# Kernel optimization log

Measured on AMD Instinct MI355X. Metric: run time of the kernel, lower is better.

## Reference

```python
import jax, jax.numpy as jnp
import numpy as np

NUM_HEAD = 16
D_MODEL = 1024


def setup_inputs() -> dict:
    key = jax.random.key(0)
    k1, k2, k3 = jax.random.split(key, 3)
    B, S = 4, 2048
    x = jax.random.normal(k1, (B, S, D_MODEL), dtype=jnp.float32)
    W_qkv = jax.random.normal(k2, (D_MODEL, 3 * D_MODEL), dtype=jnp.float32) * (D_MODEL ** -0.5)
    b_qkv = jnp.zeros((3 * D_MODEL,), dtype=jnp.float32)
    W_o = jax.random.normal(k3, (D_MODEL, D_MODEL), dtype=jnp.float32) * (D_MODEL ** -0.5)
    b_o = jnp.zeros((D_MODEL,), dtype=jnp.float32)
    return {"x": x, "W_qkv": W_qkv, "b_qkv": b_qkv, "W_o": W_o, "b_o": b_o}


def reference(x, W_qkv, b_qkv, W_o, b_o):
    B, S, dm = x.shape
    H = NUM_HEAD
    hd = dm // H
    qkv = x @ W_qkv + b_qkv                       # [B,S,3*dm]
    qkv = qkv.reshape(B, S, H, 3 * hd).transpose(0, 2, 1, 3)  # [B,H,S,3*hd]
    q, k, v = jnp.split(qkv, 3, axis=-1)          # each [B,H,S,hd]
    scale = jnp.sqrt(jnp.asarray(hd, dtype=q.dtype))
    att = jnp.einsum('bhqd,bhkd->bhqk', q, k) / scale  # [B,H,S,S]
    causal = jnp.tril(jnp.ones((S, S), dtype=bool))    # band_part(ones,-1,0)
    att = jnp.where(causal, att, -jnp.inf)             # additive 0 / -inf mask
    att = jax.nn.softmax(att, axis=-1)
    vals = jnp.einsum('bhqk,bhkd->bhqd', att, v)       # [B,H,S,hd]
    # Faithful to original: reshape WITHOUT transposing heads back (axis scramble)
    vals = vals.reshape(B, S, H * hd)
    return vals @ W_o + b_o
```

## Files before the change

kernel.cpp:

```cpp
#include <hip/hip_runtime.h>
#include <hip/hip_bf16.h>
#include <stdint.h>


typedef __attribute__((ext_vector_type(8))) __bf16 bf16x8;
typedef __attribute__((ext_vector_type(4))) float f32x4;
typedef __attribute__((ext_vector_type(16))) float f32x16;

#define AS_G __attribute__((address_space(1)))
#define AS_L __attribute__((address_space(3)))

__device__ __forceinline__ void gload_lds16(const void* g, void* s) {
  __builtin_amdgcn_global_load_lds((const AS_G void*)g, (AS_L void*)s, 16, 0, 0);
}

__device__ __forceinline__ unsigned cvt_pk_bf16(float lo, float hi) {
  unsigned r;
  asm("v_cvt_pk_bf16_f32 %0, %1, %2" : "=v"(r) : "v"(lo), "v"(hi));
  return r;
}

__global__ void cvt_bf16_kernel(const float* __restrict__ in,
                                __bf16* __restrict__ out, int n8) {
  int i = blockIdx.x * blockDim.x + threadIdx.x;
  if (i >= n8) return;
  float4 a = ((const float4*)in)[i * 2];
  float4 b = ((const float4*)in)[i * 2 + 1];
  union { __bf16 h[8]; int4 v; } u;
  u.h[0] = (__bf16)a.x; u.h[1] = (__bf16)a.y; u.h[2] = (__bf16)a.z; u.h[3] = (__bf16)a.w;
  u.h[4] = (__bf16)b.x; u.h[5] = (__bf16)b.y; u.h[6] = (__bf16)b.z; u.h[7] = (__bf16)b.w;
  ((int4*)out)[i] = u.v;
}

__global__ void cvt_T_kernel(const float* __restrict__ in,
                             __bf16* __restrict__ out, int K, int N) {
  __shared__ float tile[32][33];
  int bx = blockIdx.x;
  int by = blockIdx.y;
  int tx = threadIdx.x & 31, ty = threadIdx.x >> 5;
#pragma unroll
  for (int i = 0; i < 32; i += 8)
    tile[ty + i][tx] = in[(size_t)(by * 32 + ty + i) * N + bx * 32 + tx];
  __syncthreads();
#pragma unroll
  for (int i = 0; i < 32; i += 8)
    out[(size_t)(bx * 32 + ty + i) * K + by * 32 + tx] = (__bf16)tile[tx][ty + i];
}

template <int MODE, int NT, int MCHUNK>
__global__ __launch_bounds__(256, 2) void gemm_bt(
    const __bf16* __restrict__ A, const __bf16* __restrict__ Bt,
    const float* __restrict__ bias,
    __bf16* __restrict__ Qb, __bf16* __restrict__ Kb, __bf16* __restrict__ Vtb,
    float* __restrict__ Out) {
  __shared__ char lds[65536];
  const int tid = threadIdx.x;
  const int wave = tid >> 6, lane = tid & 63;
  const int lhi = lane >> 4, llo = lane & 15;
  const int wm = wave >> 1, wn = wave & 1;

  const int wg = blockIdx.x + blockIdx.y * gridDim.x;
  const int xcd = wg & 7, local = wg >> 3;
  const int m0 = (xcd * MCHUNK + (local & (MCHUNK - 1))) * 128;
  const int n0 = (local / MCHUNK) * 128;

  int S[2];
#pragma unroll
  for (int j = 0; j < 2; ++j) {
    const int idx = j * 256 + tid;
    const int v = idx >> 3, wl = idx & 7;
    const int wg_ = wl ^ (v & 7);
    const int r = (v << 1) | (wg_ >> 2), u2 = wg_ & 3;
    S[j] = r * 1024 + u2 * 8;
  }
  const __bf16* Asrc = A + (size_t)m0 * 1024;
  const __bf16* Bsrc = Bt + (size_t)n0 * 1024;
  const int dstw = wave * 1024;

  auto stageAB = [&](int c, int t, int ks) {
    char* ab = &lds[c * 16384 + ks * 8192];
    char* bb = &lds[32768 + c * 16384 + ks * 8192];
    const int go = t * 64 + ks * 32;
    gload_lds16(Asrc + S[0] + go, ab + dstw);
    gload_lds16(Asrc + S[1] + go, ab + 4096 + dstw);
    gload_lds16(Bsrc + S[0] + go, bb + dstw);
    gload_lds16(Bsrc + S[1] + go, bb + 4096 + dstw);
  };

  f32x4 acc[4][4];
#pragma unroll
  for (int mi = 0; mi < 4; ++mi)
#pragma unroll
    for (int nj = 0; nj < 4; ++nj) acc[mi][nj] = (f32x4){0.f, 0.f, 0.f, 0.f};

  auto aoff = [&](int c, int ks, int mi) {
    const int r = wm * 64 + mi * 16 + llo;
    const int v = r >> 1;
    const int w = ((r & 1) << 2) | lhi;
    return c * 16384 + ks * 8192 + v * 128 + ((w ^ (v & 7)) << 4);
  };
  auto boff = [&](int c, int ks, int nj) {
    const int r = wn * 64 + nj * 16 + llo;
    const int v = r >> 1;
    const int w = ((r & 1) << 2) | lhi;
    return 32768 + c * 16384 + ks * 8192 + v * 128 + ((w ^ (v & 7)) << 4);
  };

  auto phase = [&](int c, int ks, int sc, int st, int sks) {
    bf16x8 fa[4], fb[4];
#pragma unroll
    for (int mi = 0; mi < 4; ++mi) fa[mi] = *(const bf16x8*)&lds[aoff(c, ks, mi)];
#pragma unroll
    for (int nj = 0; nj < 4; ++nj) fb[nj] = *(const bf16x8*)&lds[boff(c, ks, nj)];
    stageAB(sc, st, sks);
    __builtin_amdgcn_sched_barrier(0);
    asm volatile("s_waitcnt vmcnt(8)" ::: "memory");
    __builtin_amdgcn_sched_barrier(0);
    __builtin_amdgcn_s_barrier();
    __builtin_amdgcn_s_setprio(1);
#pragma unroll
    for (int mi = 0; mi < 4; ++mi)
#pragma unroll
      for (int nj = 0; nj < 4; ++nj)
        acc[mi][nj] = __builtin_amdgcn_mfma_f32_16x16x32_bf16(fa[mi], fb[nj],
                                                              acc[mi][nj], 0, 0, 0);
    __builtin_amdgcn_s_setprio(0);
    __builtin_amdgcn_sched_barrier(0);
    __builtin_amdgcn_s_barrier();
  };

  stageAB(0, 0, 0);
  stageAB(0, 0, 1);
  stageAB(1, 1, 0);
  __builtin_amdgcn_sched_barrier(0);
  asm volatile("s_waitcnt vmcnt(8)" ::: "memory");
  __builtin_amdgcn_sched_barrier(0);
  __builtin_amdgcn_s_barrier();

  for (int it = 0; it < 8; ++it) {
    const int T = 2 * it;
    phase(0, 0, 1, (T + 1) & 15, 1);
    phase(0, 1, 0, (T + 2) & 15, 0);
    phase(1, 0, 0, (T + 2) & 15, 1);
    phase(1, 1, 1, (T + 3) & 15, 0);
  }

#pragma unroll
  for (int nj = 0; nj < 4; ++nj) {
    const int col = n0 + wn * 64 + nj * 16 + llo;
    const float bv = bias[col];
    if (MODE == 0) {
      const int h = col / 192, rem = col % 192;
#pragma unroll
      for (int mi = 0; mi < 4; ++mi) {
        const int row0 = m0 + wm * 64 + mi * 16 + lhi * 4;
        const int b = row0 >> 11;
        const int s0 = row0 & 2047;
        const int bh = b * 16 + h;
        f32x4 v = acc[mi][nj];
        if (rem < 64) {
#pragma unroll
          for (int r = 0; r < 4; ++r)
            Qb[((size_t)bh * 2048 + s0 + r) * 64 + rem] =
                (__bf16)((v[r] + bv) * 0.18033688011112042f);
        } else if (rem < 128) {
#pragma unroll
          for (int r = 0; r < 4; ++r)
            Kb[((size_t)bh * 2048 + s0 + r) * 64 + (rem - 64)] = (__bf16)(v[r] + bv);
        } else {
          union { __bf16 h4[4]; int2 v2; } u;
#pragma unroll
          for (int r = 0; r < 4; ++r) u.h4[r] = (__bf16)(v[r] + bv);
          *(int2*)&Vtb[((size_t)bh * 64 + (rem - 128)) * 2048 + s0] = u.v2;
        }
      }
    } else {
#pragma unroll
      for (int mi = 0; mi < 4; ++mi) {
        const int row0 = m0 + wm * 64 + mi * 16 + lhi * 4;
        f32x4 v = acc[mi][nj];
#pragma unroll
        for (int r = 0; r < 4; ++r)
          Out[(size_t)(row0 + r) * 1024 + col] = v[r] + bv;
      }
    }
  }
}


__device__ __forceinline__ void attn_tile(
    const __bf16* __restrict__ ksb, const __bf16* __restrict__ vsb,
    const bf16x8* qf, int kv0, int q0w, int lq, int hi,
    f32x16& o0, f32x16& o1, float& m, float& l) {
  const int r0 = lq, r1 = 32 + lq;
  const int fx = (lq & 7) ^ ((lq >> 3) << 1);
  f32x16 s0, s1;
#pragma unroll
  for (int i = 0; i < 16; ++i) { s0[i] = 0.f; s1[i] = 0.f; }
  __builtin_amdgcn_s_setprio(1);
#pragma unroll
  for (int ds = 0; ds < 4; ++ds) {
    const int bb = ((ds * 2 + hi) ^ fx) * 8;
    bf16x8 k0 = *(const bf16x8*)&ksb[r0 * 64 + bb];
    bf16x8 k1 = *(const bf16x8*)&ksb[r1 * 64 + bb];
    s0 = __builtin_amdgcn_mfma_f32_32x32x16_bf16(k0, qf[ds], s0, 0, 0, 0);
    s1 = __builtin_amdgcn_mfma_f32_32x32x16_bf16(k1, qf[ds], s1, 0, 0, 0);
  }
  __builtin_amdgcn_s_setprio(0);

  const int qg = q0w + lq;
  if (kv0 + 63 > q0w) {
#pragma unroll
    for (int reg = 0; reg < 16; ++reg) {
      const int kvl = (reg & 3) + 8 * (reg >> 2) + 4 * hi;
      if (kv0 + kvl > qg) s0[reg] = -1e30f;
      if (kv0 + 32 + kvl > qg) s1[reg] = -1e30f;
    }
  }
  float x[8];
#pragma unroll
  for (int i = 0; i < 8; ++i)
    x[i] = fmaxf(fmaxf(s0[i], s0[i + 8]), fmaxf(s1[i], s1[i + 8]));
#pragma unroll
  for (int st = 4; st; st >>= 1)
#pragma unroll
    for (int i = 0; i < st; ++i) x[i] = fmaxf(x[i], x[i + st]);
  const float mx = fmaxf(x[0], __shfl_xor(x[0], 32));

  if (!__all(mx <= m + 8.f)) {
    const float mn = fmaxf(m, mx);
    const float f = __builtin_amdgcn_exp2f(m - mn);
    m = mn;
    l *= f;
#pragma unroll
    for (int i = 0; i < 16; ++i) { o0[i] *= f; o1[i] *= f; }
  }
#pragma unroll
  for (int i = 0; i < 16; ++i) s0[i] = __builtin_amdgcn_exp2f(s0[i] - m);
#pragma unroll
  for (int i = 0; i < 16; ++i) s1[i] = __builtin_amdgcn_exp2f(s1[i] - m);
  float y[8];
#pragma unroll
  for (int i = 0; i < 8; ++i) y[i] = (s0[i] + s0[i + 8]) + (s1[i] + s1[i + 8]);
#pragma unroll
  for (int st = 4; st; st >>= 1)
#pragma unroll
    for (int i = 0; i < st; ++i) y[i] += y[i + st];
  l += y[0] + __shfl_xor(y[0], 32);

#pragma unroll
  for (int ks = 0; ks < 4; ++ks) {
    unsigned pa, pb, pc, pd;
    if (ks < 2) {
      pa = cvt_pk_bf16(s0[ks * 8 + 0], s0[ks * 8 + 1]);
      pb = cvt_pk_bf16(s0[ks * 8 + 2], s0[ks * 8 + 3]);
      pc = cvt_pk_bf16(s0[ks * 8 + 4], s0[ks * 8 + 5]);
      pd = cvt_pk_bf16(s0[ks * 8 + 6], s0[ks * 8 + 7]);
    } else {
      pa = cvt_pk_bf16(s1[(ks - 2) * 8 + 0], s1[(ks - 2) * 8 + 1]);
      pb = cvt_pk_bf16(s1[(ks - 2) * 8 + 2], s1[(ks - 2) * 8 + 3]);
      pc = cvt_pk_bf16(s1[(ks - 2) * 8 + 4], s1[(ks - 2) * 8 + 5]);
      pd = cvt_pk_bf16(s1[(ks - 2) * 8 + 6], s1[(ks - 2) * 8 + 7]);
    }
    asm volatile("v_permlane32_swap_b32 %0, %1" : "+v"(pa), "+v"(pc));
    asm volatile("v_permlane32_swap_b32 %0, %1" : "+v"(pb), "+v"(pd));
    union { unsigned u[4]; bf16x8 v; } pf;
    pf.u[0] = pa; pf.u[1] = pb; pf.u[2] = pc; pf.u[3] = pd;
    const int vb = ((ks * 2 + hi) ^ fx) * 8;
    bf16x8 v0 = *(const bf16x8*)&vsb[r0 * 64 + vb];
    bf16x8 v1 = *(const bf16x8*)&vsb[r1 * 64 + vb];
    o0 = __builtin_amdgcn_mfma_f32_32x32x16_bf16(v0, pf.v, o0, 0, 0, 0);
    o1 = __builtin_amdgcn_mfma_f32_32x32x16_bf16(v1, pf.v, o1, 0, 0, 0);
  }
}

__device__ __forceinline__ void attn_epilogue(
    __bf16* __restrict__ vals, int bh, int q0w, int lq, int hi,
    const f32x16& o0, const f32x16& o1, float l) {
  const float inv = 1.f / l;
  unsigned* outp = (unsigned*)(vals + ((size_t)bh * 2048 + q0w + lq) * 64);
#pragma unroll
  for (int n = 0; n < 2; ++n) {
#pragma unroll
    for (int g = 0; g < 2; ++g) {
      const float e0 = (n ? o1[g * 8 + 0] : o0[g * 8 + 0]) * inv;
      const float e1 = (n ? o1[g * 8 + 1] : o0[g * 8 + 1]) * inv;
      const float e2 = (n ? o1[g * 8 + 2] : o0[g * 8 + 2]) * inv;
      const float e3 = (n ? o1[g * 8 + 3] : o0[g * 8 + 3]) * inv;
      const float e4 = (n ? o1[g * 8 + 4] : o0[g * 8 + 4]) * inv;
      const float e5 = (n ? o1[g * 8 + 5] : o0[g * 8 + 5]) * inv;
      const float e6 = (n ? o1[g * 8 + 6] : o0[g * 8 + 6]) * inv;
      const float e7 = (n ? o1[g * 8 + 7] : o0[g * 8 + 7]) * inv;
      unsigned a = cvt_pk_bf16(e0, e1);
      unsigned a2 = cvt_pk_bf16(e2, e3);
      unsigned b = cvt_pk_bf16(e4, e5);
      unsigned b2 = cvt_pk_bf16(e6, e7);
      asm volatile("v_permlane32_swap_b32 %0, %1" : "+v"(a), "+v"(b));
      asm volatile("v_permlane32_swap_b32 %0, %1" : "+v"(a2), "+v"(b2));
      int4 st = {(int)a, (int)a2, (int)b, (int)b2};
      *(int4*)&outp[(n * 32 + g * 16 + hi * 8) >> 1] = st;
    }
  }
}

__global__ __launch_bounds__(256) void attn_kernel(
    const __bf16* __restrict__ Q, const __bf16* __restrict__ K,
    const __bf16* __restrict__ Vt, __bf16* __restrict__ vals) {
  __shared__ __bf16 Ks[2][4096];
  __shared__ __bf16 Vs[2][4096];
  const int tid = threadIdx.x;
  const int wave = tid >> 6, lane = tid & 63;
  const int lq = lane & 31, hi = lane >> 5;

  const int wg = blockIdx.x + (blockIdx.y << 3);
  const int wgid = (wg & 7) * 128 + (wg >> 3);
  const int local = wgid & 127;
  const int bh = (wgid >> 7) * 8 + (local & 7);
  const int qc = 15 - (local >> 3);
  const int q0w = qc * 128 + wave * 32;
  const int nt = 2 * qc + 2;

  bf16x8 qf[4];
  {
    const __bf16* qp = Q + ((size_t)bh * 2048 + q0w + lq) * 64 + hi * 8;
#pragma unroll
    for (int ds = 0; ds < 4; ++ds) qf[ds] = *(const bf16x8*)(qp + ds * 16);
  }

  f32x16 o0, o1;
#pragma unroll
  for (int i = 0; i < 16; ++i) { o0[i] = 0.f; o1[i] = 0.f; }
  float m = -3e38f, l = 0.f;

  const int sr = tid >> 3, sb_ = tid & 7;
  const int sc = (sb_ ^ ((sr & 7) ^ ((sr >> 3) << 1))) * 8;
  const __bf16* Kg0 = K + ((size_t)bh * 2048 + sr) * 64 + sc;
  const __bf16* Kg1 = Kg0 + 32 * 64;
  const __bf16* Vg0 = Vt + ((size_t)bh * 64 + sr) * 2048 + sc;
  const __bf16* Vg1 = Vg0 + 32 * 2048;
  __bf16* KsW = &Ks[0][0] + wave * 512;
  __bf16* VsW = &Vs[0][0] + wave * 512;

#define STAGE(buf, t)                                                   \
  gload_lds16(Kg0 + (size_t)(t) * 4096, KsW + (buf) * 4096);            \
  gload_lds16(Kg1 + (size_t)(t) * 4096, KsW + (buf) * 4096 + 2048);     \
  gload_lds16(Vg0 + (t) * 64, VsW + (buf) * 4096);                      \
  gload_lds16(Vg1 + (t) * 64, VsW + (buf) * 4096 + 2048);

  STAGE(0, 0);
  __syncthreads();

  for (int t = 0; t < nt; ++t) {
    const int cur = t & 1;
    if (t + 1 < nt) { STAGE(cur ^ 1, t + 1); }
    attn_tile(&Ks[cur][0], &Vs[cur][0], qf, t * 64, q0w, lq, hi, o0, o1, m, l);
    __syncthreads();
  }
#undef STAGE

  attn_epilogue(vals, bh, q0w, lq, hi, o0, o1, l);
}

extern "C" void kernel_launch(void* const* d_in, const int* in_sizes, int n_in,
                              void* d_out, int out_size, void* d_ws, size_t ws_size,
                              hipStream_t stream) {
  const float* x = (const float*)d_in[0];
  const float* Wqkv = (const float*)d_in[1];
  const float* bqkv = (const float*)d_in[2];
  const float* Wo = (const float*)d_in[3];
  const float* bo = (const float*)d_in[4];
  float* out = (float*)d_out;
  char* ws = (char*)d_ws;

  __bf16* xb  = (__bf16*)(ws);
  __bf16* Wqt = (__bf16*)(ws + 16777216);
  __bf16* Wot = (__bf16*)(ws + 23068672);
  __bf16* Qb  = (__bf16*)(ws + 25165824);
  __bf16* Kb  = (__bf16*)(ws + 41943040);
  __bf16* Vtb = (__bf16*)(ws + 58720256);
  __bf16* vals = xb;

  cvt_bf16_kernel<<<4096, 256, 0, stream>>>(x, xb, 1048576);
  cvt_T_kernel<<<dim3(96, 32), 256, 0, stream>>>(Wqkv, Wqt, 1024, 3072);
  cvt_T_kernel<<<dim3(32, 32), 256, 0, stream>>>(Wo, Wot, 1024, 1024);
  gemm_bt<0, 24, 8><<<dim3(24, 64), 256, 0, stream>>>(xb, Wqt, bqkv, Qb, Kb, Vtb, nullptr);
  attn_kernel<<<dim3(8, 128), 256, 0, stream>>>(Qb, Kb, Vtb, vals);
  gemm_bt<1, 8, 8><<<dim3(8, 64), 256, 0, stream>>>(vals, Wot, bo, nullptr, nullptr, nullptr, out);
}
```

Baseline: 171.2 us.

## Add 256x256-tile 512-thread QKV projection GEMM with quadrant-pipelined LDS staging

Replaces the 128x128-tile QKV GEMM with a dedicated kernel that uses 256x256 output tiles, 8 waves and 128KB LDS, staging A/B quadrants asynchronously while MFMAs run on other quadrants. Larger tiles halve global/LDS traffic per flop for the largest GEMM. The cost is a single workgroup per CU and 384 workgroups over the CUs, which can leave a tail wave, plus higher register pressure. The output-projection GEMM template loses its MODE parameter but keeps the same code path.

Measured after the change: 176.5 us. 1.03x slower.

```diff
diff --git a/kernel.cpp b/kernel.cpp
--- a/kernel.cpp
+++ b/kernel.cpp
@@ -47,12 +47,146 @@
     out[(size_t)(bx * 32 + ty + i) * K + by * 32 + tx] = (__bf16)tile[tx][ty + i];
 }
 
-template <int MODE, int NT, int MCHUNK>
+__global__ __launch_bounds__(512, 1) void gemm256_qkv(
+    const __bf16* __restrict__ A, const __bf16* __restrict__ Bt,
+    const float* __restrict__ bias,
+    __bf16* __restrict__ Qb, __bf16* __restrict__ Kb, __bf16* __restrict__ Vtb) {
+  __shared__ char lds[131072];
+  const int tid = threadIdx.x;
+  const int wv = tid >> 6, lane = tid & 63;
+  const int lhi = lane >> 4, llo = lane & 15;
+  const int wm = wv >> 2, wn = wv & 3;
+
+  const int wg = blockIdx.x;
+  const int xcd = wg & 7, local = wg >> 3;
+  const int m0 = (xcd * 4 + (local & 3)) * 256;
+  const int n0 = (local >> 2) * 256;
+
+  const int r_a = tid >> 3;
+  const int r_b = (tid >> 3) & 31;
+  const int u = tid & 7;
+  const __bf16* Asrc = A + (size_t)m0 * 1024;
+  const __bf16* Bsrc = Bt + (size_t)n0 * 1024;
+  const __bf16* pA[2], * pB[2];
+#pragma unroll
+  for (int j = 0; j < 2; ++j) {
+    pA[j] = Asrc + (size_t)(j * 128 + r_a) * 1024 + ((u ^ (r_a & 7)) * 8);
+    const int wnb = j * 2 + (tid >> 8);
+    pB[j] = Bsrc + (size_t)(wnb * 64 + r_b) * 1024 + ((u ^ (r_b & 7)) * 8);
+  }
+  const int wvb = wv * 1024;
+
+#define STAGE_A(c, qm, t)                                                   \
+  gload_lds16(pA[0] + (qm) * 65536 + (t) * 64,                              \
+              &lds[(c) * 32768 + (qm) * 16384 + 0 * 8192 + wvb]);           \
+  gload_lds16(pA[1] + (qm) * 65536 + (t) * 64,                              \
+              &lds[(c) * 32768 + (qm) * 16384 + 1 * 8192 + wvb]);
+#define STAGE_B(c, qn, t)                                                   \
+  gload_lds16(pB[0] + (qn) * 32768 + (t) * 64,                              \
+              &lds[65536 + (c) * 32768 + (qn) * 16384 + 0 * 8192 + wvb]);   \
+  gload_lds16(pB[1] + (qn) * 32768 + (t) * 64,                              \
+              &lds[65536 + (c) * 32768 + (qn) * 16384 + 1 * 8192 + wvb]);
+
+  f32x4 acc[8][4];
+#pragma unroll
+  for (int mi = 0; mi < 8; ++mi)
+#pragma unroll
+    for (int nj = 0; nj < 4; ++nj) acc[mi][nj] = (f32x4){0.f, 0.f, 0.f, 0.f};
+
+  int sw[2];
+#pragma unroll
+  for (int kh = 0; kh < 2; ++kh) sw[kh] = (((kh << 2) | lhi) ^ (llo & 7)) << 4;
+  const int aB = wm * 8192 + llo * 128;
+  const int bB = 65536 + wn * 4096 + llo * 128;
+
+  auto PH = [&](int c, int qm, int qn, int sel, int sc, int sq, int st) {
+    __builtin_amdgcn_s_barrier();
+    __builtin_amdgcn_sched_barrier(0);
+    bf16x8 fa[4][2], fb[2][2];
+#pragma unroll
+    for (int f = 0; f < 4; ++f)
+#pragma unroll
+      for (int kh = 0; kh < 2; ++kh)
+        fa[f][kh] = *(const bf16x8*)&lds[c * 32768 + qm * 16384 + aB + f * 2048 + sw[kh]];
+#pragma unroll
+    for (int f2 = 0; f2 < 2; ++f2)
+#pragma unroll
+      for (int kh = 0; kh < 2; ++kh)
+        fb[f2][kh] = *(const bf16x8*)&lds[c * 32768 + qn * 16384 + bB + f2 * 2048 + sw[kh]];
+    if (sel == 0) { STAGE_A(sc, sq, st); } else { STAGE_B(sc, sq, st); }
+    asm volatile("s_waitcnt lgkmcnt(0)" ::: "memory");
+    __builtin_amdgcn_sched_barrier(0);
+    __builtin_amdgcn_s_setprio(1);
+#pragma unroll
+    for (int f = 0; f < 4; ++f)
+#pragma unroll
+      for (int f2 = 0; f2 < 2; ++f2)
+#pragma unroll
+        for (int kh = 0; kh < 2; ++kh)
+          acc[qm * 4 + f][qn * 2 + f2] = __builtin_amdgcn_mfma_f32_16x16x32_bf16(
+              fa[f][kh], fb[f2][kh], acc[qm * 4 + f][qn * 2 + f2], 0, 0, 0);
+    __builtin_amdgcn_s_setprio(0);
+    __builtin_amdgcn_sched_barrier(0);
+  };
+
+  STAGE_A(0, 0, 0); STAGE_B(0, 1, 0); STAGE_A(0, 1, 0); STAGE_B(0, 0, 0);
+  STAGE_A(1, 0, 1); STAGE_B(1, 1, 1);
+
+  for (int j = 0; j < 8; ++j) {
+    const int t1 = 2 * j + 1, t2 = (2 * j + 2) & 15, t3 = (2 * j + 3) & 15;
+    __builtin_amdgcn_sched_barrier(0);
+    asm volatile("s_waitcnt vmcnt(4)" ::: "memory");
+    __builtin_amdgcn_sched_barrier(0);
+    PH(0, 0, 0, 0, 1, 1, t1);
+    PH(0, 0, 1, 1, 1, 0, t1);
+    PH(0, 1, 1, 0, 0, 0, t2);
+    PH(0, 1, 0, 1, 0, 1, t2);
+    __builtin_amdgcn_sched_barrier(0);
+    asm volatile("s_waitcnt vmcnt(4)" ::: "memory");
+    __builtin_amdgcn_sched_barrier(0);
+    PH(1, 0, 0, 0, 0, 1, t2);
+    PH(1, 0, 1, 1, 0, 0, t2);
+    PH(1, 1, 1, 0, 1, 0, t3);
+    PH(1, 1, 0, 1, 1, 1, t3);
+  }
+#undef STAGE_A
+#undef STAGE_B
+
+#pragma unroll
+  for (int nj = 0; nj < 4; ++nj) {
+    const int col = n0 + wn * 64 + nj * 16 + llo;
+    const float bv = bias[col];
+    const int h = col / 192, rem = col % 192;
+#pragma unroll
+    for (int mi = 0; mi < 8; ++mi) {
+      const int row0 = m0 + wm * 128 + mi * 16 + lhi * 4;
+      const int b = row0 >> 11;
+      const int s0 = row0 & 2047;
+      const int bh = b * 16 + h;
+      f32x4 v = acc[mi][nj];
+      if (rem < 64) {
+#pragma unroll
+        for (int r = 0; r < 4; ++r)
+          Qb[((size_t)bh * 2048 + s0 + r) * 64 + rem] =
+              (__bf16)((v[r] + bv) * 0.18033688011112042f);
+      } else if (rem < 128) {
+#pragma unroll
+        for (int r = 0; r < 4; ++r)
+          Kb[((size_t)bh * 2048 + s0 + r) * 64 + (rem - 64)] = (__bf16)(v[r] + bv);
+      } else {
+        union { __bf16 h4[4]; int2 v2; } uq;
+#pragma unroll
+        for (int r = 0; r < 4; ++r) uq.h4[r] = (__bf16)(v[r] + bv);
+        *(int2*)&Vtb[((size_t)bh * 64 + (rem - 128)) * 2048 + s0] = uq.v2;
+      }
+    }
+  }
+}
+
+template <int NT, int MCHUNK>
 __global__ __launch_bounds__(256, 2) void gemm_bt(
     const __bf16* __restrict__ A, const __bf16* __restrict__ Bt,
-    const float* __restrict__ bias,
-    __bf16* __restrict__ Qb, __bf16* __restrict__ Kb, __bf16* __restrict__ Vtb,
-    float* __restrict__ Out) {
+    const float* __restrict__ bias, float* __restrict__ Out) {
   __shared__ char lds[65536];
   const int tid = threadIdx.x;
   const int wave = tid >> 6, lane = tid & 63;
@@ -149,40 +283,13 @@
   for (int nj = 0; nj < 4; ++nj) {
     const int col = n0 + wn * 64 + nj * 16 + llo;
     const float bv = bias[col];
-    if (MODE == 0) {
-      const int h = col / 192, rem = col % 192;
-#pragma unroll
-      for (int mi = 0; mi < 4; ++mi) {
-        const int row0 = m0 + wm * 64 + mi * 16 + lhi * 4;
-        const int b = row0 >> 11;
-        const int s0 = row0 & 2047;
-        const int bh = b * 16 + h;
-        f32x4 v = acc[mi][nj];
-        if (rem < 64) {
-#pragma unroll
-          for (int r = 0; r < 4; ++r)
-            Qb[((size_t)bh * 2048 + s0 + r) * 64 + rem] =
-                (__bf16)((v[r] + bv) * 0.18033688011112042f);
-        } else if (rem < 128) {
-#pragma unroll
-          for (int r = 0; r < 4; ++r)
-            Kb[((size_t)bh * 2048 + s0 + r) * 64 + (rem - 64)] = (__bf16)(v[r] + bv);
-        } else {
-          union { __bf16 h4[4]; int2 v2; } u;
-#pragma unroll
-          for (int r = 0; r < 4; ++r) u.h4[r] = (__bf16)(v[r] + bv);
-          *(int2*)&Vtb[((size_t)bh * 64 + (rem - 128)) * 2048 + s0] = u.v2;
-        }
-      }
-    } else {
-#pragma unroll
-      for (int mi = 0; mi < 4; ++mi) {
-        const int row0 = m0 + wm * 64 + mi * 16 + lhi * 4;
-        f32x4 v = acc[mi][nj];
-#pragma unroll
-        for (int r = 0; r < 4; ++r)
-          Out[(size_t)(row0 + r) * 1024 + col] = v[r] + bv;
-      }
+#pragma unroll
+    for (int mi = 0; mi < 4; ++mi) {
+      const int row0 = m0 + wm * 64 + mi * 16 + lhi * 4;
+      f32x4 v = acc[mi][nj];
+#pragma unroll
+      for (int r = 0; r < 4; ++r)
+        Out[(size_t)(row0 + r) * 1024 + col] = v[r] + bv;
     }
   }
 }
@@ -383,7 +490,7 @@
   cvt_bf16_kernel<<<4096, 256, 0, stream>>>(x, xb, 1048576);
   cvt_T_kernel<<<dim3(96, 32), 256, 0, stream>>>(Wqkv, Wqt, 1024, 3072);
   cvt_T_kernel<<<dim3(32, 32), 256, 0, stream>>>(Wo, Wot, 1024, 1024);
-  gemm_bt<0, 24, 8><<<dim3(24, 64), 256, 0, stream>>>(xb, Wqt, bqkv, Qb, Kb, Vtb, nullptr);
+  gemm256_qkv<<<384, 512, 0, stream>>>(xb, Wqt, bqkv, Qb, Kb, Vtb);
   attn_kernel<<<dim3(8, 128), 256, 0, stream>>>(Qb, Kb, Vtb, vals);
-  gemm_bt<1, 8, 8><<<dim3(8, 64), 256, 0, stream>>>(vals, Wot, bo, nullptr, nullptr, nullptr, out);
-}
+  gemm_bt<8, 8><<<dim3(8, 64), 256, 0, stream>>>(vals, Wot, bo, out);
+}
```

## Use 256x128 tile, 512-thread kernel for QKV projection GEMM

Applied to the files above, without the earlier changes.

Adds a dedicated QKV GEMM kernel with 256-row by 128-column tiles, 8 waves per block and 96KB of LDS, replacing the 128x128 templated GEMM for the first projection. Larger M tiles halve the number of B-tile reloads per output and improve arithmetic intensity per LDS byte. The trade-off is one block per CU (launch_bounds 512,1), which gives less latency hiding, and a grid of 768 blocks whose mapping to the 8 XCDs must be correct. The output GEMM template loses its MODE parameter.

Result: faster. 166.2 us (-2.9%).

```diff
diff --git a/kernel.cpp b/kernel.cpp
--- a/kernel.cpp
+++ b/kernel.cpp
@@ -47,12 +47,140 @@
     out[(size_t)(bx * 32 + ty + i) * K + by * 32 + tx] = (__bf16)tile[tx][ty + i];
 }
 
-template <int MODE, int NT, int MCHUNK>
+__global__ __launch_bounds__(512, 1) void gemm256_qkv(
+    const __bf16* __restrict__ A, const __bf16* __restrict__ Bt,
+    const float* __restrict__ bias,
+    __bf16* __restrict__ Qb, __bf16* __restrict__ Kb, __bf16* __restrict__ Vtb) {
+  __shared__ char lds[98304];
+  const int tid = threadIdx.x;
+  const int wv = tid >> 6, lane = tid & 63;
+  const int lhi = lane >> 4, llo = lane & 15;
+  const int wm = wv >> 1, wn = wv & 1;
+
+  const int wg = blockIdx.x;
+  const int xcd = wg & 7, local = wg >> 3;
+  const int m0 = (xcd * 4 + (local & 3)) * 256;
+  const int n0 = (local >> 2) * 128;
+
+  int SA[2], SB;
+#pragma unroll
+  for (int j = 0; j < 2; ++j) {
+    const int idx = j * 512 + tid;
+    const int v = idx >> 3, wl = idx & 7;
+    const int wg_ = wl ^ (v & 7);
+    SA[j] = ((v << 1) | (wg_ >> 2)) * 1024 + (wg_ & 3) * 8;
+  }
+  {
+    const int v = tid >> 3, wl = tid & 7;
+    const int wg_ = wl ^ (v & 7);
+    SB = ((v << 1) | (wg_ >> 2)) * 1024 + (wg_ & 3) * 8;
+  }
+  const __bf16* Asrc = A + (size_t)m0 * 1024;
+  const __bf16* Bsrc = Bt + (size_t)n0 * 1024;
+  const int wvb = wv * 1024;
+
+#define STAGE_AB(c, t, ks)                                                  \
+  gload_lds16(Asrc + SA[0] + (t) * 64 + (ks) * 32,                          \
+              &lds[(c) * 32768 + (ks) * 16384 + wvb]);                      \
+  gload_lds16(Asrc + SA[1] + (t) * 64 + (ks) * 32,                          \
+              &lds[(c) * 32768 + (ks) * 16384 + 8192 + wvb]);               \
+  gload_lds16(Bsrc + SB + (t) * 64 + (ks) * 32,                             \
+              &lds[65536 + (c) * 16384 + (ks) * 8192 + wvb]);
+
+  f32x4 acc[4][4];
+#pragma unroll
+  for (int mi = 0; mi < 4; ++mi)
+#pragma unroll
+    for (int nj = 0; nj < 4; ++nj) acc[mi][nj] = (f32x4){0.f, 0.f, 0.f, 0.f};
+
+  auto aoff = [&](int c, int ks, int f) {
+    const int r = wm * 64 + f * 16 + llo;
+    const int v = r >> 1;
+    const int w = ((r & 1) << 2) | lhi;
+    return c * 32768 + ks * 16384 + v * 128 + ((w ^ (v & 7)) << 4);
+  };
+  auto boff = [&](int c, int ks, int f2) {
+    const int r = wn * 64 + f2 * 16 + llo;
+    const int v = r >> 1;
+    const int w = ((r & 1) << 2) | lhi;
+    return 65536 + c * 16384 + ks * 8192 + v * 128 + ((w ^ (v & 7)) << 4);
+  };
+
+  auto PH = [&](int c, int ks, int sc, int st, int sks) {
+    bf16x8 fa[4], fb[4];
+#pragma unroll
+    for (int f = 0; f < 4; ++f) fa[f] = *(const bf16x8*)&lds[aoff(c, ks, f)];
+#pragma unroll
+    for (int f2 = 0; f2 < 4; ++f2) fb[f2] = *(const bf16x8*)&lds[boff(c, ks, f2)];
+    STAGE_AB(sc, st, sks);
+    __builtin_amdgcn_sched_barrier(0);
+    __builtin_amdgcn_s_barrier();
+    asm volatile("s_waitcnt lgkmcnt(0)" ::: "memory");
+    __builtin_amdgcn_sched_barrier(0);
+    __builtin_amdgcn_s_setprio(1);
+#pragma unroll
+    for (int mi = 0; mi < 4; ++mi)
+#pragma unroll
+      for (int nj = 0; nj < 4; ++nj)
+        acc[mi][nj] = __builtin_amdgcn_mfma_f32_16x16x32_bf16(fa[mi], fb[nj],
+                                                              acc[mi][nj], 0, 0, 0);
+    __builtin_amdgcn_s_setprio(0);
+    __builtin_amdgcn_sched_barrier(0);
+    asm volatile("s_waitcnt vmcnt(6)" ::: "memory");
+    __builtin_amdgcn_s_barrier();
+  };
+
+  STAGE_AB(0, 0, 0);
+  STAGE_AB(0, 0, 1);
+  STAGE_AB(1, 1, 0);
+  __builtin_amdgcn_sched_barrier(0);
+  asm volatile("s_waitcnt vmcnt(6)" ::: "memory");
+  __builtin_amdgcn_s_barrier();
+
+  for (int j = 0; j < 8; ++j) {
+    const int t1 = 2 * j + 1, t2 = (2 * j + 2) & 15, t3 = (2 * j + 3) & 15;
+    PH(0, 0, 1, t1, 1);
+    PH(0, 1, 0, t2, 0);
+    PH(1, 0, 0, t2, 1);
+    PH(1, 1, 1, t3, 0);
+  }
+#undef STAGE_AB
+
+#pragma unroll
+  for (int nj = 0; nj < 4; ++nj) {
+    const int col = n0 + wn * 64 + nj * 16 + llo;
+    const float bv = bias[col];
+    const int h = col / 192, rem = col % 192;
+#pragma unroll
+    for (int mi = 0; mi < 4; ++mi) {
+      const int row0 = m0 + wm * 64 + mi * 16 + lhi * 4;
+      const int b = row0 >> 11;
+      const int s0 = row0 & 2047;
+      const int bh = b * 16 + h;
+      f32x4 v = acc[mi][nj];
+      if (rem < 64) {
+#pragma unroll
+        for (int r = 0; r < 4; ++r)
+          Qb[((size_t)bh * 2048 + s0 + r) * 64 + rem] =
+              (__bf16)((v[r] + bv) * 0.18033688011112042f);
+      } else if (rem < 128) {
+#pragma unroll
+        for (int r = 0; r < 4; ++r)
+          Kb[((size_t)bh * 2048 + s0 + r) * 64 + (rem - 64)] = (__bf16)(v[r] + bv);
+      } else {
+        union { __bf16 h4[4]; int2 v2; } uq;
+#pragma unroll
+        for (int r = 0; r < 4; ++r) uq.h4[r] = (__bf16)(v[r] + bv);
+        *(int2*)&Vtb[((size_t)bh * 64 + (rem - 128)) * 2048 + s0] = uq.v2;
+      }
+    }
+  }
+}
+
+template <int NT, int MCHUNK>
 __global__ __launch_bounds__(256, 2) void gemm_bt(
     const __bf16* __restrict__ A, const __bf16* __restrict__ Bt,
-    const float* __restrict__ bias,
-    __bf16* __restrict__ Qb, __bf16* __restrict__ Kb, __bf16* __restrict__ Vtb,
-    float* __restrict__ Out) {
+    const float* __restrict__ bias, float* __restrict__ Out) {
   __shared__ char lds[65536];
   const int tid = threadIdx.x;
   const int wave = tid >> 6, lane = tid & 63;
@@ -149,40 +277,13 @@
   for (int nj = 0; nj < 4; ++nj) {
     const int col = n0 + wn * 64 + nj * 16 + llo;
     const float bv = bias[col];
-    if (MODE == 0) {
-      const int h = col / 192, rem = col % 192;
-#pragma unroll
-      for (int mi = 0; mi < 4; ++mi) {
-        const int row0 = m0 + wm * 64 + mi * 16 + lhi * 4;
-        const int b = row0 >> 11;
-        const int s0 = row0 & 2047;
-        const int bh = b * 16 + h;
-        f32x4 v = acc[mi][nj];
-        if (rem < 64) {
-#pragma unroll
-          for (int r = 0; r < 4; ++r)
-            Qb[((size_t)bh * 2048 + s0 + r) * 64 + rem] =
-                (__bf16)((v[r] + bv) * 0.18033688011112042f);
-        } else if (rem < 128) {
-#pragma unroll
-          for (int r = 0; r < 4; ++r)
-            Kb[((size_t)bh * 2048 + s0 + r) * 64 + (rem - 64)] = (__bf16)(v[r] + bv);
-        } else {
-          union { __bf16 h4[4]; int2 v2; } u;
-#pragma unroll
-          for (int r = 0; r < 4; ++r) u.h4[r] = (__bf16)(v[r] + bv);
-          *(int2*)&Vtb[((size_t)bh * 64 + (rem - 128)) * 2048 + s0] = u.v2;
-        }
-      }
-    } else {
-#pragma unroll
-      for (int mi = 0; mi < 4; ++mi) {
-        const int row0 = m0 + wm * 64 + mi * 16 + lhi * 4;
-        f32x4 v = acc[mi][nj];
-#pragma unroll
-        for (int r = 0; r < 4; ++r)
-          Out[(size_t)(row0 + r) * 1024 + col] = v[r] + bv;
-      }
+#pragma unroll
+    for (int mi = 0; mi < 4; ++mi) {
+      const int row0 = m0 + wm * 64 + mi * 16 + lhi * 4;
+      f32x4 v = acc[mi][nj];
+#pragma unroll
+      for (int r = 0; r < 4; ++r)
+        Out[(size_t)(row0 + r) * 1024 + col] = v[r] + bv;
     }
   }
 }
@@ -383,7 +484,7 @@
   cvt_bf16_kernel<<<4096, 256, 0, stream>>>(x, xb, 1048576);
   cvt_T_kernel<<<dim3(96, 32), 256, 0, stream>>>(Wqkv, Wqt, 1024, 3072);
   cvt_T_kernel<<<dim3(32, 32), 256, 0, stream>>>(Wo, Wot, 1024, 1024);
-  gemm_bt<0, 24, 8><<<dim3(24, 64), 256, 0, stream>>>(xb, Wqt, bqkv, Qb, Kb, Vtb, nullptr);
+  gemm256_qkv<<<768, 512, 0, stream>>>(xb, Wqt, bqkv, Qb, Kb, Vtb);
   attn_kernel<<<dim3(8, 128), 256, 0, stream>>>(Qb, Kb, Vtb, vals);
-  gemm_bt<1, 8, 8><<<dim3(8, 64), 256, 0, stream>>>(vals, Wot, bo, nullptr, nullptr, nullptr, out);
-}
+  gemm_bt<8, 8><<<dim3(8, 64), 256, 0, stream>>>(vals, Wot, bo, out);
+}
```
